# Kernel tuning notes

Measured on AMD Instinct MI355X. Metric: run time of the kernel, lower is better.

## Reference

```python
import jax, jax.numpy as jnp
import numpy as np
from jax import lax

D_MODEL = 1024
D_STATE = 16
D_CONV = 4
EXPAND = 2
D_INNER = EXPAND * D_MODEL  # 2048
DT_RANK = (D_MODEL + 15) // 16  # 64
EPS = 1e-5


def setup_inputs() -> dict:
    key = jax.random.key(0)
    ks = jax.random.split(key, 10)
    B, L = 2, 2048
    x = jax.random.normal(ks[0], (B, L, D_MODEL), dtype=jnp.float32)
    s = 0.02
    W_in = jax.random.normal(ks[1], (D_MODEL, 2 * D_INNER), dtype=jnp.float32) * s
    conv_w = jax.random.normal(ks[2], (D_INNER, 1, D_CONV), dtype=jnp.float32) * 0.3
    conv_b = jnp.zeros((D_INNER,), dtype=jnp.float32)
    W_xproj = jax.random.normal(ks[3], (D_INNER, DT_RANK + 2 * D_STATE), dtype=jnp.float32) * s
    W_dt = jax.random.normal(ks[4], (DT_RANK, D_INNER), dtype=jnp.float32) * s
    b_dt = jax.random.normal(ks[5], (D_INNER,), dtype=jnp.float32) * 0.1
    # canonical S4D-real init: A_log = log(1..d_state) broadcast over channels
    A_log = jnp.broadcast_to(jnp.log(jnp.arange(1, D_STATE + 1, dtype=jnp.float32)), (D_INNER, D_STATE))
    D = jnp.ones((D_INNER,), dtype=jnp.float32)
    W_out = jax.random.normal(ks[6], (D_INNER, D_MODEL), dtype=jnp.float32) * s
    return {
        'x': x,
        'ln_w': jnp.ones((D_MODEL,), dtype=jnp.float32),
        'ln_b': jnp.zeros((D_MODEL,), dtype=jnp.float32),
        'W_in': W_in, 'conv_w': conv_w, 'conv_b': conv_b,
        'W_xproj': W_xproj, 'W_dt': W_dt, 'b_dt': b_dt,
        'A_log': A_log, 'D': D, 'W_out': W_out,
    }


def _layernorm(x, w, b):
    mu = jnp.mean(x, axis=-1, keepdims=True)
    var = jnp.mean(jnp.square(x - mu), axis=-1, keepdims=True)
    return (x - mu) * lax.rsqrt(var + EPS) * w + b


def _mamba_forward(normed, W_in, conv_w, conv_b, W_xproj, W_dt, b_dt, A_log, D, W_out):
    Bsz, L, _ = normed.shape
    xz = normed @ W_in                       # (B, L, 2*d_inner)
    u, z = jnp.split(xz, 2, axis=-1)         # each (B, L, d_inner)
    # depthwise causal conv over time
    uc = lax.conv_general_dilated(
        jnp.swapaxes(u, 1, 2), conv_w,       # (B, d_inner, L), (d_inner, 1, k)
        window_strides=(1,), padding=[(D_CONV - 1, 0)],
        feature_group_count=D_INNER,
        dimension_numbers=('NCH', 'OIH', 'NCH'))
    uc = uc + conv_b[None, :, None]
    u = jax.nn.silu(jnp.swapaxes(uc, 1, 2))  # (B, L, d_inner)
    # input-dependent dt, B, C
    dbc = u @ W_xproj                        # (B, L, dt_rank + 2*d_state)
    dt = dbc[..., :DT_RANK]
    Bm = dbc[..., DT_RANK:DT_RANK + D_STATE]
    Cm = dbc[..., DT_RANK + D_STATE:]
    delta = jax.nn.softplus(dt @ W_dt + b_dt)  # (B, L, d_inner)
    A = -jnp.exp(A_log)                        # (d_inner, d_state)

    def step(h, inp):
        delta_t, u_t, B_t, C_t = inp           # (B,d), (B,d), (B,n), (B,n)
        dA = jnp.exp(delta_t[:, :, None] * A)  # (B, d, n)
        h = dA * h + (delta_t * u_t)[:, :, None] * B_t[:, None, :]
        y = jnp.einsum('bdn,bn->bd', h, C_t)
        return h, y

    tm = lambda a: jnp.swapaxes(a, 0, 1)       # time-major
    h0 = jnp.zeros((Bsz, D_INNER, D_STATE), dtype=normed.dtype)
    _, ys = lax.scan(step, h0, (tm(delta), tm(u), tm(Bm), tm(Cm)))
    y = jnp.swapaxes(ys, 0, 1) + u * D         # (B, L, d_inner)
    y = y * jax.nn.silu(z)
    return y @ W_out                            # (B, L, d_model)


def reference(x, ln_w, ln_b, W_in, conv_w, conv_b, W_xproj, W_dt, b_dt, A_log, D, W_out):
    normed = _layernorm(x, ln_w, ln_b)
    ssm_out = _mamba_forward(normed, W_in, conv_w, conv_b, W_xproj, W_dt, b_dt, A_log, D, W_out)
    # dropout is identity at inference
    return x + ssm_out
```

## Files before the change

kernel.cpp:

```cpp
#include <hip/hip_runtime.h>
#include <math.h>

#define D_MODEL 1024
#define D_INNER 2048
#define D_STATE 16
#define DT_RANK 64
#define LSEQ    2048
#define NTOK    4096
#define SCH     32
#define SCL     (LSEQ / SCH)
#define LOG2E   1.44269504088896f
#define XKS     4
#define XKC     (D_INNER / XKS)

typedef short bf16x8 __attribute__((ext_vector_type(8)));
typedef float f32x4  __attribute__((ext_vector_type(4)));

__device__ __forceinline__ unsigned bf16_rne(float v) {
    unsigned u = __float_as_uint(v);
    return (u + 0x7FFFu + ((u >> 16) & 1u)) >> 16;
}
__device__ __forceinline__ void split_hi_lo(float v, short& h, short& l) {
    unsigned hb = bf16_rne(v);
    h = (short)hb;
    float r = v - __uint_as_float(hb << 16);
    l = (short)bf16_rne(r);
}

__global__ __launch_bounds__(256) void ln_kernel(const float* __restrict__ x,
                                                 const float* __restrict__ w,
                                                 const float* __restrict__ b,
                                                 short* __restrict__ nh,
                                                 short* __restrict__ nl)
{
    int t = blockIdx.x;
    const float4* xr = (const float4*)(x + (size_t)t * D_MODEL);
    float4 v = xr[threadIdx.x];
    float s  = v.x + v.y + v.z + v.w;
    float s2 = v.x*v.x + v.y*v.y + v.z*v.z + v.w*v.w;
    for (int off = 32; off > 0; off >>= 1) {
        s  += __shfl_down(s, off);
        s2 += __shfl_down(s2, off);
    }
    __shared__ float red[8];
    int wid = threadIdx.x >> 6, lane = threadIdx.x & 63;
    if (lane == 0) { red[wid] = s; red[4 + wid] = s2; }
    __syncthreads();
    if (threadIdx.x == 0) {
        float a = red[0] + red[1] + red[2] + red[3];
        float c = red[4] + red[5] + red[6] + red[7];
        red[0] = a * (1.f / (float)D_MODEL);
        red[4] = c * (1.f / (float)D_MODEL);
    }
    __syncthreads();
    float mu  = red[0];
    float var = red[4] - mu * mu;
    float rs  = rsqrtf(var + 1e-5f);
    float4 wv = ((const float4*)w)[threadIdx.x];
    float4 bv = ((const float4*)b)[threadIdx.x];
    float4 o;
    o.x = (v.x - mu) * rs * wv.x + bv.x;
    o.y = (v.y - mu) * rs * wv.y + bv.y;
    o.z = (v.z - mu) * rs * wv.z + bv.z;
    o.w = (v.w - mu) * rs * wv.w + bv.w;
    short4 h4, l4;
    split_hi_lo(o.x, h4.x, l4.x);
    split_hi_lo(o.y, h4.y, l4.y);
    split_hi_lo(o.z, h4.z, l4.z);
    split_hi_lo(o.w, h4.w, l4.w);
    size_t off = (size_t)t * D_MODEL + threadIdx.x * 4;
    *(short4*)&nh[off] = h4;
    *(short4*)&nl[off] = l4;
}

__global__ __launch_bounds__(256) void cvtT_k(const float* __restrict__ W,
                                              short* __restrict__ Th,
                                              short* __restrict__ Tl,
                                              int R, int Cc)
{
    __shared__ float t[64][65];
    int rr = threadIdx.x >> 4;
    int cc = (threadIdx.x & 15) << 2;
    int r0 = blockIdx.y * 64, c0 = blockIdx.x * 64;
#pragma unroll
    for (int s = 0; s < 4; ++s) {
        float4 v = *(const float4*)&W[(size_t)(r0 + rr + 16*s) * Cc + c0 + cc];
        t[rr+16*s][cc+0] = v.x; t[rr+16*s][cc+1] = v.y;
        t[rr+16*s][cc+2] = v.z; t[rr+16*s][cc+3] = v.w;
    }
    __syncthreads();
#pragma unroll
    for (int s = 0; s < 4; ++s) {
        int orow = rr + 16*s;
        short4 h4, l4;
        split_hi_lo(t[cc+0][orow], h4.x, l4.x);
        split_hi_lo(t[cc+1][orow], h4.y, l4.y);
        split_hi_lo(t[cc+2][orow], h4.z, l4.z);
        split_hi_lo(t[cc+3][orow], h4.w, l4.w);
        size_t off = (size_t)(c0 + orow) * R + r0 + cc;
        *(short4*)&Th[off] = h4;
        *(short4*)&Tl[off] = l4;
    }
}

template<int EPI>
__global__ __launch_bounds__(256) void mgemm_k(const short* __restrict__ Ah,
                                               const short* __restrict__ Al,
                                               const short* __restrict__ Bh,
                                               const short* __restrict__ Bl,
                                               float* __restrict__ C, int ldc,
                                               int K, const float* __restrict__ aux)
{
    __shared__ short lds[2][4][128 * 32];

    int tid  = threadIdx.x;
    int w    = tid >> 6;
    int lane = tid & 63;
    int wr   = w >> 1, wc = w & 1;
    int row0 = blockIdx.y * 128;
    int col0 = blockIdx.x * 128;

    const short* gA = (w & 1) ? Al : Ah;
    const short* gB = (w & 1) ? Bl : Bh;
    const short* g  = (w & 2) ? gB : gA;
    int obase       = (w & 2) ? col0 : row0;
    const short* gtile = g + (size_t)obase * K;

    int fr = lane & 15;
    int kg = lane >> 4;

    f32x4 acc[4][4] = {};

#if __has_builtin(__builtin_amdgcn_global_load_lds)
#define STAGE(bufi, kk)                                                          \
    {                                                                            \
        _Pragma("unroll")                                                        \
        for (int i = 0; i < 8; ++i) {                                            \
            const short* src = gtile + (size_t)(i * 16 + fr) * K + (kk) + kg * 8;\
            __builtin_amdgcn_global_load_lds(                                    \
                (const __attribute__((address_space(1))) void*)src,              \
                (__attribute__((address_space(3))) void*)&lds[bufi][w][i * 512], \
                16, 0, 0);                                                       \
        }                                                                        \
    }

    STAGE(0, 0);
    __syncthreads();
    int buf = 0;
    for (int k0 = 0; k0 < K; k0 += 32) {
        if (k0 + 32 < K) STAGE(buf ^ 1, k0 + 32);

        bf16x8 a_h[4], a_l[4], b_h[4], b_l[4];
#pragma unroll
        for (int m = 0; m < 4; ++m) {
            int ra = ((wr * 4 + m) * 4 + kg) * 128 + fr * 8;
            int rb = ((wc * 4 + m) * 4 + kg) * 128 + fr * 8;
            a_h[m] = *(const bf16x8*)&lds[buf][0][ra];
            a_l[m] = *(const bf16x8*)&lds[buf][1][ra];
            b_h[m] = *(const bf16x8*)&lds[buf][2][rb];
            b_l[m] = *(const bf16x8*)&lds[buf][3][rb];
        }
#pragma unroll
        for (int m = 0; m < 4; ++m)
#pragma unroll
            for (int n = 0; n < 4; ++n)
                acc[m][n] = __builtin_amdgcn_mfma_f32_16x16x32_bf16(a_h[m], b_h[n], acc[m][n], 0, 0, 0);
#pragma unroll
        for (int m = 0; m < 4; ++m)
#pragma unroll
            for (int n = 0; n < 4; ++n)
                acc[m][n] = __builtin_amdgcn_mfma_f32_16x16x32_bf16(a_l[m], b_h[n], acc[m][n], 0, 0, 0);
#pragma unroll
        for (int m = 0; m < 4; ++m)
#pragma unroll
            for (int n = 0; n < 4; ++n)
                acc[m][n] = __builtin_amdgcn_mfma_f32_16x16x32_bf16(a_h[m], b_l[n], acc[m][n], 0, 0, 0);

        __syncthreads();
        buf ^= 1;
    }
#undef STAGE
#else
    int srow  = lane >> 2;
    int skc   = lane & 3;
    int swoff = skc * 128 + srow * 8;
    for (int k0 = 0; k0 < K; k0 += 32) {
        bf16x8 stg[8];
#pragma unroll
        for (int i = 0; i < 8; ++i)
            stg[i] = *(const bf16x8*)(gtile + (size_t)(i * 16 + srow) * K + k0 + skc * 8);
        __syncthreads();
#pragma unroll
        for (int i = 0; i < 8; ++i)
            *(bf16x8*)&lds[0][w][i * 512 + swoff] = stg[i];
        __syncthreads();
        bf16x8 a_h[4], a_l[4], b_h[4], b_l[4];
#pragma unroll
        for (int m = 0; m < 4; ++m) {
            int ra = ((wr * 4 + m) * 4 + kg) * 128 + fr * 8;
            int rb = ((wc * 4 + m) * 4 + kg) * 128 + fr * 8;
            a_h[m] = *(const bf16x8*)&lds[0][0][ra];
            a_l[m] = *(const bf16x8*)&lds[0][1][ra];
            b_h[m] = *(const bf16x8*)&lds[0][2][rb];
            b_l[m] = *(const bf16x8*)&lds[0][3][rb];
        }
#pragma unroll
        for (int m = 0; m < 4; ++m)
#pragma unroll
            for (int n = 0; n < 4; ++n) {
                acc[m][n] = __builtin_amdgcn_mfma_f32_16x16x32_bf16(a_h[m], b_h[n], acc[m][n], 0, 0, 0);
                acc[m][n] = __builtin_amdgcn_mfma_f32_16x16x32_bf16(a_l[m], b_h[n], acc[m][n], 0, 0, 0);
                acc[m][n] = __builtin_amdgcn_mfma_f32_16x16x32_bf16(a_h[m], b_l[n], acc[m][n], 0, 0, 0);
            }
    }
#endif

#pragma unroll
    for (int m = 0; m < 4; ++m) {
        int row = row0 + wr * 64 + m * 16 + kg * 4;
#pragma unroll
        for (int n = 0; n < 4; ++n) {
            int col = col0 + wc * 64 + n * 16 + fr;
#pragma unroll
            for (int j = 0; j < 4; ++j) {
                size_t off = (size_t)(row + j) * ldc + col;
                float v = acc[m][n][j];
                if (EPI == 2) v += aux[off];
                C[off] = v;
            }
        }
    }
}

#define TBM 128
#define TBN 128
#define TBK 16

template<int EPI>
__global__ __launch_bounds__(256) void sgemm128_k(const float* __restrict__ A, int lda,
                                                  const float* __restrict__ B, int ldb,
                                                  float* __restrict__ C, int ldc,
                                                  int K, const float* __restrict__ aux)
{
    __shared__ float As[TBK][TBM + 4];
    __shared__ float Bs[TBK][TBN + 4];

    int tid  = threadIdx.x;
    int row0 = blockIdx.y * TBM;
    int col0 = blockIdx.x * TBN;

    int arow = tid >> 2;
    int acol = (tid & 3) << 2;
    int brow = tid >> 5;
    int bcol = (tid & 31) << 2;

    int tr = tid >> 4;
    int tc = tid & 15;

    float acc[8][8] = {};

    for (int k0 = 0; k0 < K; k0 += TBK) {
        float4 a0 = *(const float4*)(A + (size_t)(row0 + arow)      * lda + k0 + acol);
        float4 a1 = *(const float4*)(A + (size_t)(row0 + arow + 64) * lda + k0 + acol);
        float4 b0 = *(const float4*)(B + (size_t)(k0 + brow)     * ldb + col0 + bcol);
        float4 b1 = *(const float4*)(B + (size_t)(k0 + brow + 8) * ldb + col0 + bcol);
        __syncthreads();
        As[acol + 0][arow] = a0.x;
        As[acol + 1][arow] = a0.y;
        As[acol + 2][arow] = a0.z;
        As[acol + 3][arow] = a0.w;
        As[acol + 0][arow + 64] = a1.x;
        As[acol + 1][arow + 64] = a1.y;
        As[acol + 2][arow + 64] = a1.z;
        As[acol + 3][arow + 64] = a1.w;
        *(float4*)&Bs[brow][bcol]     = b0;
        *(float4*)&Bs[brow + 8][bcol] = b1;
        __syncthreads();
#pragma unroll
        for (int kk = 0; kk < TBK; ++kk) {
            float4 x0 = *(const float4*)&As[kk][tr << 2];
            float4 x1 = *(const float4*)&As[kk][(tr << 2) + 64];
            float4 y0 = *(const float4*)&Bs[kk][tc << 2];
            float4 y1 = *(const float4*)&Bs[kk][(tc << 2) + 64];
            float xa[8] = {x0.x, x0.y, x0.z, x0.w, x1.x, x1.y, x1.z, x1.w};
            float yb[8] = {y0.x, y0.y, y0.z, y0.w, y1.x, y1.y, y1.z, y1.w};
#pragma unroll
            for (int i = 0; i < 8; ++i)
#pragma unroll
                for (int j = 0; j < 8; ++j)
                    acc[i][j] = fmaf(xa[i], yb[j], acc[i][j]);
        }
    }

#pragma unroll
    for (int ih = 0; ih < 2; ++ih) {
#pragma unroll
        for (int i = 0; i < 4; ++i) {
            int r = row0 + (tr << 2) + ih * 64 + i;
#pragma unroll
            for (int jh = 0; jh < 2; ++jh) {
                int c = col0 + (tc << 2) + jh * 64;
                size_t off = (size_t)r * ldc + c;
                float4 v = *(const float4*)&acc[ih * 4 + i][jh * 4];
                if (EPI == 1) {
                    float4 bb = *(const float4*)(aux + c);
                    float t0;
                    t0 = v.x + bb.x; v.x = fmaxf(t0, 0.f) + log1pf(expf(-fabsf(t0)));
                    t0 = v.y + bb.y; v.y = fmaxf(t0, 0.f) + log1pf(expf(-fabsf(t0)));
                    t0 = v.z + bb.z; v.z = fmaxf(t0, 0.f) + log1pf(expf(-fabsf(t0)));
                    t0 = v.w + bb.w; v.w = fmaxf(t0, 0.f) + log1pf(expf(-fabsf(t0)));
                } else if (EPI == 2) {
                    float4 rr = *(const float4*)(aux + off);
                    v.x += rr.x; v.y += rr.y; v.z += rr.z; v.w += rr.w;
                }
                *(float4*)(C + off) = v;
            }
        }
    }
}

__global__ __launch_bounds__(256) void xproj_k(const float* __restrict__ A,
                                               const float* __restrict__ W,
                                               float* __restrict__ part)
{
    int row = blockIdx.x * 256 + threadIdx.x;
    int cg  = blockIdx.y;
    int ks  = blockIdx.z;
    const float4* a4 = (const float4*)(A + (size_t)row * D_INNER + ks * XKC);
    const float* w = W + (size_t)ks * XKC * 96 + cg * 8;
    float acc[8] = {};
#pragma unroll 2
    for (int k4 = 0; k4 < XKC / 4; ++k4) {
        float4 av = a4[k4];
        const float* wk = w + (size_t)k4 * 4 * 96;
        float a0 = av.x, a1 = av.y, a2 = av.z, a3 = av.w;
#pragma unroll
        for (int kk = 0; kk < 4; ++kk) {
            float ak = (kk == 0) ? a0 : (kk == 1) ? a1 : (kk == 2) ? a2 : a3;
            float4 w0 = *(const float4*)(wk + (size_t)kk * 96);
            float4 w1 = *(const float4*)(wk + (size_t)kk * 96 + 4);
            acc[0] = fmaf(ak, w0.x, acc[0]);
            acc[1] = fmaf(ak, w0.y, acc[1]);
            acc[2] = fmaf(ak, w0.z, acc[2]);
            acc[3] = fmaf(ak, w0.w, acc[3]);
            acc[4] = fmaf(ak, w1.x, acc[4]);
            acc[5] = fmaf(ak, w1.y, acc[5]);
            acc[6] = fmaf(ak, w1.z, acc[6]);
            acc[7] = fmaf(ak, w1.w, acc[7]);
        }
    }
    float* p = part + ((size_t)ks * NTOK + row) * 96 + cg * 8;
    *(float4*)p       = *(float4*)&acc[0];
    *(float4*)(p + 4) = *(float4*)&acc[4];
}

__global__ __launch_bounds__(256) void xreduce_k(const float* __restrict__ part,
                                                 float* __restrict__ dbc)
{
    int i = blockIdx.x * 256 + threadIdx.x;
    const float4* p = (const float4*)part;
    float4 s0 = p[i];
    float4 s1 = p[i + 98304];
    float4 s2 = p[i + 2 * 98304];
    float4 s3 = p[i + 3 * 98304];
    float4 s;
    s.x = (s0.x + s1.x) + (s2.x + s3.x);
    s.y = (s0.y + s1.y) + (s2.y + s3.y);
    s.z = (s0.z + s1.z) + (s2.z + s3.z);
    s.w = (s0.w + s1.w) + (s2.w + s3.w);
    ((float4*)dbc)[i] = s;
}

__global__ __launch_bounds__(256) void conv_silu_kernel(const float* __restrict__ xz,
                                                        const float* __restrict__ conv_w,
                                                        const float* __restrict__ conv_b,
                                                        float* __restrict__ uc)
{
    int idx = blockIdx.x * 256 + threadIdx.x;
    if (idx >= NTOK * D_INNER) return;
    int d  = idx & (D_INNER - 1);
    int bl = idx >> 11;
    int l  = bl & (LSEQ - 1);
    float4 w = ((const float4*)conv_w)[d];
    float acc = conv_b[d];
    if (l >= 3) acc += w.x * xz[(size_t)(bl - 3) * (2 * D_INNER) + d];
    if (l >= 2) acc += w.y * xz[(size_t)(bl - 2) * (2 * D_INNER) + d];
    if (l >= 1) acc += w.z * xz[(size_t)(bl - 1) * (2 * D_INNER) + d];
    acc += w.w * xz[(size_t)bl * (2 * D_INNER) + d];
    uc[idx] = acc / (1.f + expf(-acc));
}

__global__ __launch_bounds__(256) void scan1_kernel(const float* __restrict__ delta,
                                                    const float* __restrict__ uc,
                                                    const float* __restrict__ dbc,
                                                    const float* __restrict__ A_log,
                                                    float* __restrict__ carry_A,
                                                    float* __restrict__ carry_h)
{
    __shared__ float Bs[SCL][16];
    int tid = threadIdx.x;
    int chunk = blockIdx.x, dg = blockIdx.y, b = blockIdx.z;
    int d = dg * 256 + tid;
    int rb0 = b * LSEQ + chunk * SCL;

    for (int i = tid; i < SCL * 16; i += 256) {
        int l = i >> 4, n = i & 15;
        Bs[l][n] = dbc[(size_t)(rb0 + l) * 96 + DT_RANK + n];
    }
    __syncthreads();

    float A2[16];
#pragma unroll
    for (int q = 0; q < 4; ++q) {
        float4 a = *(const float4*)&A_log[d * D_STATE + q * 4];
        A2[q*4+0] = -expf(a.x) * LOG2E;
        A2[q*4+1] = -expf(a.y) * LOG2E;
        A2[q*4+2] = -expf(a.z) * LOG2E;
        A2[q*4+3] = -expf(a.w) * LOG2E;
    }

    float h[16];
#pragma unroll
    for (int n = 0; n < 16; ++n) h[n] = 0.f;
    float sdv = 0.f;

    const float* dp = delta + (size_t)rb0 * D_INNER + d;
    const float* up = uc    + (size_t)rb0 * D_INNER + d;

    float dv = dp[0], uv = up[0];
    for (int l = 0; l < SCL; ++l) {
        float dvn = 0.f, uvn = 0.f;
        if (l + 1 < SCL) { dvn = dp[(l+1) * D_INNER]; uvn = up[(l+1) * D_INNER]; }
        float du = dv * uv;
        sdv += dv;
#pragma unroll
        for (int q = 0; q < 4; ++q) {
            float4 bq = *(const float4*)&Bs[l][q * 4];
            h[q*4+0] = fmaf(exp2f(dv * A2[q*4+0]), h[q*4+0], du * bq.x);
            h[q*4+1] = fmaf(exp2f(dv * A2[q*4+1]), h[q*4+1], du * bq.y);
            h[q*4+2] = fmaf(exp2f(dv * A2[q*4+2]), h[q*4+2], du * bq.z);
            h[q*4+3] = fmaf(exp2f(dv * A2[q*4+3]), h[q*4+3], du * bq.w);
        }
        dv = dvn; uv = uvn;
    }

    size_t cb = (((size_t)chunk * 2 + b) * D_INNER + d) * D_STATE;
#pragma unroll
    for (int q = 0; q < 4; ++q) {
        float4 ap, hh;
        ap.x = exp2f(sdv * A2[q*4+0]); ap.y = exp2f(sdv * A2[q*4+1]);
        ap.z = exp2f(sdv * A2[q*4+2]); ap.w = exp2f(sdv * A2[q*4+3]);
        hh.x = h[q*4+0]; hh.y = h[q*4+1]; hh.z = h[q*4+2]; hh.w = h[q*4+3];
        *(float4*)&carry_A[cb + q * 4] = ap;
        *(float4*)&carry_h[cb + q * 4] = hh;
    }
}

__global__ __launch_bounds__(256) void scan2_kernel(const float* __restrict__ carry_A,
                                                    float* __restrict__ carry_h)
{
    int idx = blockIdx.x * 256 + threadIdx.x;
    float h = 0.f;
#pragma unroll
    for (int c = 0; c < SCH; ++c) {
        size_t a = (size_t)c * (2 * D_INNER * D_STATE) + idx;
        float Ap = carry_A[a];
        float he = carry_h[a];
        carry_h[a] = h;
        h = fmaf(Ap, h, he);
    }
}

__global__ __launch_bounds__(256) void scan3_kernel(const float* __restrict__ delta,
                                                    const float* __restrict__ uc,
                                                    const float* __restrict__ dbc,
                                                    const float* __restrict__ xz,
                                                    const float* __restrict__ A_log,
                                                    const float* __restrict__ Dp,
                                                    const float* __restrict__ carry_h,
                                                    short* __restrict__ ygh,
                                                    short* __restrict__ ygl)
{
    __shared__ float Bs[SCL][16];
    __shared__ float Cs[SCL][16];
    int tid = threadIdx.x;
    int chunk = blockIdx.x, dg = blockIdx.y, b = blockIdx.z;
    int d = dg * 256 + tid;
    int rb0 = b * LSEQ + chunk * SCL;

    for (int i = tid; i < SCL * 32; i += 256) {
        int l = i >> 5, o = i & 31;
        float v = dbc[(size_t)(rb0 + l) * 96 + DT_RANK + o];
        if (o < 16) Bs[l][o] = v; else Cs[l][o - 16] = v;
    }
    __syncthreads();

    float A2[16];
#pragma unroll
    for (int q = 0; q < 4; ++q) {
        float4 a = *(const float4*)&A_log[d * D_STATE + q * 4];
        A2[q*4+0] = -expf(a.x) * LOG2E;
        A2[q*4+1] = -expf(a.y) * LOG2E;
        A2[q*4+2] = -expf(a.z) * LOG2E;
        A2[q*4+3] = -expf(a.w) * LOG2E;
    }
    float Dv = Dp[d];

    float h[16];
    size_t cb = (((size_t)chunk * 2 + b) * D_INNER + d) * D_STATE;
#pragma unroll
    for (int q = 0; q < 4; ++q) {
        float4 hh = *(const float4*)&carry_h[cb + q * 4];
        h[q*4+0] = hh.x; h[q*4+1] = hh.y; h[q*4+2] = hh.z; h[q*4+3] = hh.w;
    }

    const float* dp = delta + (size_t)rb0 * D_INNER + d;
    const float* up = uc    + (size_t)rb0 * D_INNER + d;
    const float* zp = xz    + (size_t)rb0 * (2 * D_INNER) + D_INNER + d;
    short* yhp = ygh + (size_t)rb0 * D_INNER + d;
    short* ylp = ygl + (size_t)rb0 * D_INNER + d;

    float dv = dp[0], uv = up[0], zv = zp[0];
    for (int l = 0; l < SCL; ++l) {
        float dvn = 0.f, uvn = 0.f, zvn = 0.f;
        if (l + 1 < SCL) {
            dvn = dp[(l+1) * D_INNER];
            uvn = up[(l+1) * D_INNER];
            zvn = zp[(size_t)(l+1) * (2 * D_INNER)];
        }
        float du = dv * uv;
        float y = 0.f;
#pragma unroll
        for (int q = 0; q < 4; ++q) {
            float4 bq = *(const float4*)&Bs[l][q * 4];
            float4 cq = *(const float4*)&Cs[l][q * 4];
            h[q*4+0] = fmaf(exp2f(dv * A2[q*4+0]), h[q*4+0], du * bq.x);
            h[q*4+1] = fmaf(exp2f(dv * A2[q*4+1]), h[q*4+1], du * bq.y);
            h[q*4+2] = fmaf(exp2f(dv * A2[q*4+2]), h[q*4+2], du * bq.z);
            h[q*4+3] = fmaf(exp2f(dv * A2[q*4+3]), h[q*4+3], du * bq.w);
            y = fmaf(h[q*4+0], cq.x, y);
            y = fmaf(h[q*4+1], cq.y, y);
            y = fmaf(h[q*4+2], cq.z, y);
            y = fmaf(h[q*4+3], cq.w, y);
        }
        float yd  = fmaf(uv, Dv, y);
        float val = yd * (zv / (1.f + expf(-zv)));
        short hh, ll;
        split_hi_lo(val, hh, ll);
        yhp[l * D_INNER] = hh;
        ylp[l * D_INNER] = ll;
        dv = dvn; uv = uvn; zv = zvn;
    }
}

__global__ __launch_bounds__(256) void scan_kernel(const float* __restrict__ delta,
                                                   const float* __restrict__ uc,
                                                   const float* __restrict__ dbc,
                                                   const float* __restrict__ xz,
                                                   const float* __restrict__ A_log,
                                                   const float* __restrict__ Dp,
                                                   short* __restrict__ ygh,
                                                   short* __restrict__ ygl)
{
    int tid = threadIdx.x;
    int g = tid >> 4, n = tid & 15;
    int bid = blockIdx.x;
    int b = bid >> 7;
    int d = (bid & 127) * 16 + g;
    float Adn = -expf(A_log[d * D_STATE + n]);
    float Dv  = Dp[d];
    float h = 0.f;
    size_t rowb = (size_t)b * LSEQ;

    float dv = delta[rowb * D_INNER + d];
    float uv = uc[rowb * D_INNER + d];
    float Bv = dbc[rowb * 96 + DT_RANK + n];
    float Cv = dbc[rowb * 96 + DT_RANK + D_STATE + n];

    for (int l = 0; l < LSEQ; ++l) {
        float dv_n = 0.f, uv_n = 0.f, Bv_n = 0.f, Cv_n = 0.f;
        if (l + 1 < LSEQ) {
            size_t r = rowb + l + 1;
            dv_n = delta[r * D_INNER + d];
            uv_n = uc[r * D_INNER + d];
            Bv_n = dbc[r * 96 + DT_RANK + n];
            Cv_n = dbc[r * 96 + DT_RANK + D_STATE + n];
        }
        float dA = expf(dv * Adn);
        h = fmaf(dA, h, dv * uv * Bv);
        float p = h * Cv;
        p += __shfl_xor(p, 1);
        p += __shfl_xor(p, 2);
        p += __shfl_xor(p, 4);
        p += __shfl_xor(p, 8);
        if (n == 0) {
            size_t r = rowb + l;
            float zv = xz[r * (2 * D_INNER) + D_INNER + d];
            float y  = fmaf(uv, Dv, p);
            float val = y * (zv / (1.f + expf(-zv)));
            short hh, ll;
            split_hi_lo(val, hh, ll);
            ygh[r * D_INNER + d] = hh;
            ygl[r * D_INNER + d] = ll;
        }
        dv = dv_n; uv = uv_n; Bv = Bv_n; Cv = Cv_n;
    }
}

extern "C" void kernel_launch(void* const* d_in, const int* in_sizes, int n_in,
                              void* d_out, int out_size, void* d_ws, size_t ws_size,
                              hipStream_t stream)
{
    const float* x      = (const float*)d_in[0];
    const float* ln_w   = (const float*)d_in[1];
    const float* ln_b   = (const float*)d_in[2];
    const float* W_in   = (const float*)d_in[3];
    const float* conv_w = (const float*)d_in[4];
    const float* conv_b = (const float*)d_in[5];
    const float* W_xprj = (const float*)d_in[6];
    const float* W_dt   = (const float*)d_in[7];
    const float* b_dt   = (const float*)d_in[8];
    const float* A_log  = (const float*)d_in[9];
    const float* Dp     = (const float*)d_in[10];
    const float* W_out  = (const float*)d_in[11];
    float* out = (float*)d_out;

    float* xz    = (float*)d_ws;
    float* uc    = xz    + (size_t)NTOK * 2 * D_INNER;
    float* dbc   = uc    + (size_t)NTOK * D_INNER;
    float* delta = dbc   + (size_t)NTOK * 96;
    short* s0    = (short*)(delta + (size_t)NTOK * D_INNER);
    short* nh    = s0;
    short* nl    = nh   + (size_t)NTOK * D_MODEL;
    short* wiTh  = nl   + (size_t)NTOK * D_MODEL;
    short* wiTl  = wiTh + (size_t)(2 * D_INNER) * D_MODEL;
    short* ygh   = s0;
    short* ygl   = ygh  + (size_t)NTOK * D_INNER;
    short* woTh  = ygl  + (size_t)NTOK * D_INNER;
    short* woTl  = woTh + (size_t)D_MODEL * D_INNER;
    float* xpart = (float*)s0;
    float* carry_A = (float*)(s0 + (size_t)20971520);
    float* carry_h = carry_A + (size_t)2 * D_INNER * D_STATE * SCH;

    size_t needed_base = (size_t)135790592 + (size_t)41943040;
    size_t needed_fast = needed_base + (size_t)2 * 2 * D_INNER * D_STATE * SCH * 4;
    if (ws_size < needed_base) return;
    bool fast_scan = (ws_size >= needed_fast);

    cvtT_k<<<dim3(2 * D_INNER / 64, D_MODEL / 64), 256, 0, stream>>>(W_in, wiTh, wiTl, D_MODEL, 2 * D_INNER);
    cvtT_k<<<dim3(D_MODEL / 64, D_INNER / 64), 256, 0, stream>>>(W_out, woTh, woTl, D_INNER, D_MODEL);
    ln_kernel<<<NTOK, 256, 0, stream>>>(x, ln_w, ln_b, nh, nl);
    mgemm_k<0><<<dim3(2 * D_INNER / 128, NTOK / 128), 256, 0, stream>>>(
        nh, nl, wiTh, wiTl, xz, 2 * D_INNER, D_MODEL, nullptr);
    conv_silu_kernel<<<(NTOK * D_INNER) / 256, 256, 0, stream>>>(xz, conv_w, conv_b, uc);
    xproj_k<<<dim3(NTOK / 256, 12, XKS), 256, 0, stream>>>(uc, W_xprj, xpart);
    xreduce_k<<<(NTOK * 96 / 4) / 256, 256, 0, stream>>>(xpart, dbc);
    sgemm128_k<1><<<dim3(D_INNER / TBN, NTOK / TBM), 256, 0, stream>>>(
        dbc, 96, W_dt, D_INNER, delta, D_INNER, DT_RANK, b_dt);
    if (fast_scan) {
        scan1_kernel<<<dim3(SCH, D_INNER / 256, 2), 256, 0, stream>>>(
            delta, uc, dbc, A_log, carry_A, carry_h);
        scan2_kernel<<<(2 * D_INNER * D_STATE) / 256, 256, 0, stream>>>(carry_A, carry_h);
        scan3_kernel<<<dim3(SCH, D_INNER / 256, 2), 256, 0, stream>>>(
            delta, uc, dbc, xz, A_log, Dp, carry_h, ygh, ygl);
    } else {
        scan_kernel<<<256, 256, 0, stream>>>(delta, uc, dbc, xz, A_log, Dp, ygh, ygl);
    }
    mgemm_k<2><<<dim3(D_MODEL / 128, NTOK / 128), 256, 0, stream>>>(
        ygh, ygl, woTh, woTl, out, D_MODEL, D_INNER, x);
}
```

Measured before the change: 569.3 us.

## Split-K output GEMM with reduction kernel, setprio around MFMA, 4-step conv

The output projection GEMM now splits K across two z-slices, writing partial sums into the delta buffer, and a new reduction kernel adds them together with the residual. This raises the block count from 256 to 512 so more of the GPU's compute units are occupied. The MFMA section is bracketed with s_setprio to favour waves in the math phase. The conv+SiLU kernel now computes four consecutive timesteps per thread, reusing the seven loaded inputs instead of reloading overlapping ones. The cost is extra partial-sum traffic through global memory and one more kernel launch.

```diff
diff --git a/kernel.cpp b/kernel.cpp
--- a/kernel.cpp
+++ b/kernel.cpp
@@ -109,7 +109,8 @@
                                                const short* __restrict__ Bh,
                                                const short* __restrict__ Bl,
                                                float* __restrict__ C, int ldc,
-                                               int K, const float* __restrict__ aux)
+                                               int Kiter, int lda,
+                                               const float* __restrict__ aux)
 {
     __shared__ short lds[2][4][128 * 32];
 
@@ -119,12 +120,14 @@
     int wr   = w >> 1, wc = w & 1;
     int row0 = blockIdx.y * 128;
     int col0 = blockIdx.x * 128;
+    int kz   = blockIdx.z;
 
     const short* gA = (w & 1) ? Al : Ah;
     const short* gB = (w & 1) ? Bl : Bh;
     const short* g  = (w & 2) ? gB : gA;
     int obase       = (w & 2) ? col0 : row0;
-    const short* gtile = g + (size_t)obase * K;
+    const short* gtile = g + (size_t)obase * lda + (size_t)kz * Kiter;
+    C += (size_t)kz * NTOK * ldc;
 
     int fr = lane & 15;
     int kg = lane >> 4;
@@ -132,23 +135,23 @@
     f32x4 acc[4][4] = {};
 
 #if __has_builtin(__builtin_amdgcn_global_load_lds)
-#define STAGE(bufi, kk)                                                          \
-    {                                                                            \
-        _Pragma("unroll")                                                        \
-        for (int i = 0; i < 8; ++i) {                                            \
-            const short* src = gtile + (size_t)(i * 16 + fr) * K + (kk) + kg * 8;\
-            __builtin_amdgcn_global_load_lds(                                    \
-                (const __attribute__((address_space(1))) void*)src,              \
-                (__attribute__((address_space(3))) void*)&lds[bufi][w][i * 512], \
-                16, 0, 0);                                                       \
-        }                                                                        \
+#define STAGE(bufi, kk)                                                            \
+    {                                                                              \
+        _Pragma("unroll")                                                          \
+        for (int i = 0; i < 8; ++i) {                                              \
+            const short* src = gtile + (size_t)(i * 16 + fr) * lda + (kk) + kg * 8;\
+            __builtin_amdgcn_global_load_lds(                                      \
+                (const __attribute__((address_space(1))) void*)src,                \
+                (__attribute__((address_space(3))) void*)&lds[bufi][w][i * 512],   \
+                16, 0, 0);                                                         \
+        }                                                                          \
     }
 
     STAGE(0, 0);
     __syncthreads();
     int buf = 0;
-    for (int k0 = 0; k0 < K; k0 += 32) {
-        if (k0 + 32 < K) STAGE(buf ^ 1, k0 + 32);
+    for (int k0 = 0; k0 < Kiter; k0 += 32) {
+        if (k0 + 32 < Kiter) STAGE(buf ^ 1, k0 + 32);
 
         bf16x8 a_h[4], a_l[4], b_h[4], b_l[4];
 #pragma unroll
@@ -160,6 +163,7 @@
             b_h[m] = *(const bf16x8*)&lds[buf][2][rb];
             b_l[m] = *(const bf16x8*)&lds[buf][3][rb];
         }
+        __builtin_amdgcn_s_setprio(1);
 #pragma unroll
         for (int m = 0; m < 4; ++m)
 #pragma unroll
@@ -175,6 +179,7 @@
 #pragma unroll
             for (int n = 0; n < 4; ++n)
                 acc[m][n] = __builtin_amdgcn_mfma_f32_16x16x32_bf16(a_h[m], b_l[n], acc[m][n], 0, 0, 0);
+        __builtin_amdgcn_s_setprio(0);
 
         __syncthreads();
         buf ^= 1;
@@ -184,11 +189,11 @@
     int srow  = lane >> 2;
     int skc   = lane & 3;
     int swoff = skc * 128 + srow * 8;
-    for (int k0 = 0; k0 < K; k0 += 32) {
+    for (int k0 = 0; k0 < Kiter; k0 += 32) {
         bf16x8 stg[8];
 #pragma unroll
         for (int i = 0; i < 8; ++i)
-            stg[i] = *(const bf16x8*)(gtile + (size_t)(i * 16 + srow) * K + k0 + skc * 8);
+            stg[i] = *(const bf16x8*)(gtile + (size_t)(i * 16 + srow) * lda + k0 + skc * 8);
         __syncthreads();
 #pragma unroll
         for (int i = 0; i < 8; ++i)
@@ -230,6 +235,22 @@
             }
         }
     }
+}
+
+__global__ __launch_bounds__(256) void outred_k(const float* __restrict__ x,
+                                                const float* __restrict__ part,
+                                                float* __restrict__ out)
+{
+    int i = blockIdx.x * 256 + threadIdx.x;
+    float4 xv = ((const float4*)x)[i];
+    float4 p0 = ((const float4*)part)[i];
+    float4 p1 = ((const float4*)part)[i + (NTOK * D_MODEL / 4)];
+    float4 o;
+    o.x = xv.x + p0.x + p1.x;
+    o.y = xv.y + p0.y + p1.y;
+    o.z = xv.z + p0.z + p1.z;
+    o.w = xv.w + p0.w + p1.w;
+    ((float4*)out)[i] = o;
 }
 
 #define TBM 128
@@ -377,17 +398,25 @@
                                                         float* __restrict__ uc)
 {
     int idx = blockIdx.x * 256 + threadIdx.x;
-    if (idx >= NTOK * D_INNER) return;
-    int d  = idx & (D_INNER - 1);
-    int bl = idx >> 11;
-    int l  = bl & (LSEQ - 1);
+    if (idx >= NTOK * D_INNER / 4) return;
+    int d   = idx & (D_INNER - 1);
+    int g4  = idx >> 11;
+    int b   = g4 / (LSEQ / 4);
+    int l0  = (g4 % (LSEQ / 4)) * 4;
+    int bl0 = b * LSEQ + l0;
     float4 w = ((const float4*)conv_w)[d];
-    float acc = conv_b[d];
-    if (l >= 3) acc += w.x * xz[(size_t)(bl - 3) * (2 * D_INNER) + d];
-    if (l >= 2) acc += w.y * xz[(size_t)(bl - 2) * (2 * D_INNER) + d];
-    if (l >= 1) acc += w.z * xz[(size_t)(bl - 1) * (2 * D_INNER) + d];
-    acc += w.w * xz[(size_t)bl * (2 * D_INNER) + d];
-    uc[idx] = acc / (1.f + expf(-acc));
+    float bb = conv_b[d];
+    float t[7];
+#pragma unroll
+    for (int k = 0; k < 7; ++k) {
+        int l = l0 - 3 + k;
+        t[k] = (l >= 0) ? xz[(size_t)(bl0 - 3 + k) * (2 * D_INNER) + d] : 0.f;
+    }
+#pragma unroll
+    for (int j = 0; j < 4; ++j) {
+        float acc = bb + w.x * t[j] + w.y * t[j+1] + w.z * t[j+2] + w.w * t[j+3];
+        uc[(size_t)(bl0 + j) * D_INNER + d] = acc / (1.f + expf(-acc));
+    }
 }
 
 __global__ __launch_bounds__(256) void scan1_kernel(const float* __restrict__ delta,
@@ -639,6 +668,7 @@
     short* woTh  = ygl  + (size_t)NTOK * D_INNER;
     short* woTl  = woTh + (size_t)D_MODEL * D_INNER;
     float* xpart = (float*)s0;
+    float* gpart = delta;
     float* carry_A = (float*)(s0 + (size_t)20971520);
     float* carry_h = carry_A + (size_t)2 * D_INNER * D_STATE * SCH;
 
@@ -650,9 +680,9 @@
     cvtT_k<<<dim3(2 * D_INNER / 64, D_MODEL / 64), 256, 0, stream>>>(W_in, wiTh, wiTl, D_MODEL, 2 * D_INNER);
     cvtT_k<<<dim3(D_MODEL / 64, D_INNER / 64), 256, 0, stream>>>(W_out, woTh, woTl, D_INNER, D_MODEL);
     ln_kernel<<<NTOK, 256, 0, stream>>>(x, ln_w, ln_b, nh, nl);
-    mgemm_k<0><<<dim3(2 * D_INNER / 128, NTOK / 128), 256, 0, stream>>>(
-        nh, nl, wiTh, wiTl, xz, 2 * D_INNER, D_MODEL, nullptr);
-    conv_silu_kernel<<<(NTOK * D_INNER) / 256, 256, 0, stream>>>(xz, conv_w, conv_b, uc);
+    mgemm_k<0><<<dim3(2 * D_INNER / 128, NTOK / 128, 1), 256, 0, stream>>>(
+        nh, nl, wiTh, wiTl, xz, 2 * D_INNER, D_MODEL, D_MODEL, nullptr);
+    conv_silu_kernel<<<(NTOK * D_INNER / 4) / 256, 256, 0, stream>>>(xz, conv_w, conv_b, uc);
     xproj_k<<<dim3(NTOK / 256, 12, XKS), 256, 0, stream>>>(uc, W_xprj, xpart);
     xreduce_k<<<(NTOK * 96 / 4) / 256, 256, 0, stream>>>(xpart, dbc);
     sgemm128_k<1><<<dim3(D_INNER / TBN, NTOK / TBM), 256, 0, stream>>>(
@@ -666,6 +696,7 @@
     } else {
         scan_kernel<<<256, 256, 0, stream>>>(delta, uc, dbc, xz, A_log, Dp, ygh, ygl);
     }
-    mgemm_k<2><<<dim3(D_MODEL / 128, NTOK / 128), 256, 0, stream>>>(
-        ygh, ygl, woTh, woTl, out, D_MODEL, D_INNER, x);
-}
+    mgemm_k<0><<<dim3(D_MODEL / 128, NTOK / 128, 2), 256, 0, stream>>>(
+        ygh, ygl, woTh, woTl, gpart, D_MODEL, D_INNER / 2, D_INNER, nullptr);
+    outred_k<<<(NTOK * D_MODEL / 4) / 256, 256, 0, stream>>>(x, gpart, out);
+}
```

Result: faster. 540.8 us (-5.0%).
